# Performance work log

Hardware: AMD Instinct MI355X
Metric: run time of the kernel (lower is better)

Reference implementation:

```python
import jax, jax.numpy as jnp
import numpy as np

B, T, D, H = 4, 4096, 256, 64  # batch, seq, DIM_EMBEDDING (fixed constant), head_size


def setup_inputs() -> dict:
    key = jax.random.key(0)
    ks = jax.random.split(key, 6)
    x = jax.random.normal(ks[0], (B, T, D), dtype=jnp.float32)
    scale = jnp.float32(0.02)
    Wq = jax.random.normal(ks[1], (D, H), dtype=jnp.float32) * scale
    Wk = jax.random.normal(ks[2], (D, H), dtype=jnp.float32) * scale
    Wv = jax.random.normal(ks[3], (D, H), dtype=jnp.float32) * scale
    two_pi = jnp.float32(2.0 * np.pi)
    angles_x = jax.random.uniform(ks[4], (T, H // 4), dtype=jnp.float32, maxval=two_pi)
    angles_y = jax.random.uniform(ks[5], (T, H // 4), dtype=jnp.float32, maxval=two_pi)
    return {"x": x, "Wq": Wq, "Wk": Wk, "Wv": Wv, "angles_x": angles_x, "angles_y": angles_y}


def _rope_half(v, freqs):
    # v: (B, T, H/2) real; freqs: (T, H/4) complex64 (unit phasors)
    b, t, h = v.shape
    vc = v.astype(jnp.float32).reshape(b, t, h // 2, 2)
    vz = jax.lax.complex(vc[..., 0], vc[..., 1])         # (B, T, H/4)
    rz = vz * freqs[None]                                 # complex multiply per position
    out = jnp.stack([jnp.real(rz), jnp.imag(rz)], axis=-1)
    return out.reshape(b, t, h)


def _rope2d(v, fx, fy):
    vx, vy = jnp.split(v, 2, axis=-1)
    return jnp.concatenate([_rope_half(vx, fx), _rope_half(vy, fy)], axis=-1)


def reference(x, Wq, Wk, Wv, angles_x, angles_y):
    # complex unit phasors e^{i*theta}
    fx = jax.lax.complex(jnp.cos(angles_x), jnp.sin(angles_x))
    fy = jax.lax.complex(jnp.cos(angles_y), jnp.sin(angles_y))
    # original apply_rotary_embeddings is wrapped in @torch.no_grad -> detached
    q = jax.lax.stop_gradient(_rope2d(x @ Wq, fx, fy))
    k = jax.lax.stop_gradient(_rope2d(x @ Wk, fx, fy))
    v = x @ Wv
    C = x.shape[-1]  # NOTE: source scales by embedding dim (256), not head dim
    wei = jnp.einsum('bth,bsh->bts', q, k) / jnp.sqrt(jnp.float32(C))
    softwei = jax.nn.softmax(wei, axis=-1)  # no causal mask in source
    out = jnp.einsum('bts,bsh->bth', softwei, v)
    return out
```

## Files before the change

kernel.cpp:

```cpp
#include <hip/hip_runtime.h>

#define B_ 4
#define T_ 4096
#define D_ 256
#define H_ 64
#define NBT (B_ * T_)
#define NBTH (B_ * T_ * H_)

typedef __bf16 bf16x8 __attribute__((ext_vector_type(8)));
typedef float f32x4 __attribute__((ext_vector_type(4)));

__device__ __forceinline__ unsigned short f2bf(float f) {
  union { float f; unsigned int u; } v; v.f = f;
  unsigned int u = v.u;
  return (unsigned short)((u + 0x7fffu + ((u >> 16) & 1u)) >> 16);
}

#if __has_builtin(__builtin_amdgcn_cvt_pk_bf16_f32)
typedef __bf16 bf16x2_t __attribute__((ext_vector_type(2)));
__device__ __forceinline__ unsigned int pk2(float a, float b) {
  union { bf16x2_t v; unsigned int u; } c;
  c.v = __builtin_amdgcn_cvt_pk_bf16_f32(a, b);
  return c.u;
}
#else
__device__ __forceinline__ unsigned int pk2(float a, float b) {
  return (unsigned int)f2bf(a) | ((unsigned int)f2bf(b) << 16);
}
#endif

#if __has_builtin(__builtin_amdgcn_exp2f)
#define EXP2(x) __builtin_amdgcn_exp2f(x)
#else
#define EXP2(x) exp2f(x)
#endif

#define QSCALE 0.09016844f


__global__ __launch_bounds__(256) void prep_w_kernel(
    const float* __restrict__ Wq, const float* __restrict__ Wk,
    const float* __restrict__ Wv, unsigned short* __restrict__ wt) {
  const int m = blockIdx.x >> 2;
  const int cp = blockIdx.x & 3;
  const float* W = (m == 0) ? Wq : (m == 1) ? Wk : Wv;
  const float scale = (m == 0) ? QSCALE : 1.f;
  __shared__ __align__(16) unsigned short tile[64][72];
  int h = threadIdx.x & 63, dq = threadIdx.x >> 6;
  const int d0 = cp * 64;
  for (int dl = dq; dl < 64; dl += 4)
    tile[h][dl] = f2bf(W[(d0 + dl) * H_ + h] * scale);
  __syncthreads();
  int ht = threadIdx.x >> 6;
  int lane = threadIdx.x & 63, quad = lane >> 4, l16 = lane & 15;
#pragma unroll
  for (int cl = 0; cl < 2; ++cl) {
    int c = cp * 2 + cl;
    bf16x8 v = *(const bf16x8*)&tile[ht * 16 + l16][cl * 32 + quad * 8];
    *(bf16x8*)&wt[(((m * 4 + ht) * 8 + c) << 9) + lane * 8] = v;
  }
}

__global__ __launch_bounds__(192) void qkv_kernel(
    const float* __restrict__ x, const unsigned short* __restrict__ wt,
    const float* __restrict__ axg, const float* __restrict__ ayg,
    unsigned short* __restrict__ qo, unsigned short* __restrict__ ko,
    unsigned short* __restrict__ vt) {
  const int row0g = blockIdx.x * 16;
  const int tid = threadIdx.x;
  const int w = tid / 64, lane = tid & 63, quad = lane >> 4, l16 = lane & 15;

  __shared__ unsigned short xs[16][264];
  __shared__ unsigned short qkt[2][16][72];
  __shared__ unsigned short vsh[64][16];

  const float4* xb = (const float4*)(x + (size_t)row0g * D_);
  for (int i = tid; i < 1024; i += 192) {
    float4 v = xb[i];
    int r = i >> 6, c4 = (i & 63) << 2;
    *(unsigned int*)&xs[r][c4] = pk2(v.x, v.y);
    *(unsigned int*)&xs[r][c4 + 2] = pk2(v.z, v.w);
  }
  __syncthreads();

  bf16x8 xf[8];
#pragma unroll
  for (int c = 0; c < 8; ++c)
    xf[c] = *(const bf16x8*)&xs[l16][c * 32 + quad * 8];

  const unsigned short* wb = wt + (((size_t)w * 4) * 8 << 9);
  f32x4 acc[4];
#pragma unroll
  for (int ht = 0; ht < 4; ++ht) acc[ht] = (f32x4){0.f, 0.f, 0.f, 0.f};
#pragma unroll
  for (int c = 0; c < 8; ++c) {
#pragma unroll
    for (int ht = 0; ht < 4; ++ht) {
      bf16x8 wf = *(const bf16x8*)&wb[((ht * 8 + c) << 9) + lane * 8];
      acc[ht] = __builtin_amdgcn_mfma_f32_16x16x32_bf16(xf[c], wf, acc[ht],
                                                        0, 0, 0);
    }
  }

  const int row0loc = row0g & (T_ - 1);
  if (w < 2) {
    const float sgn = (l16 & 1) ? 1.f : -1.f;
#pragma unroll
    for (int ht = 0; ht < 4; ++ht) {
      int hh = ht * 16 + l16;
      int pidx = (hh & 31) >> 1;
      const float* ab = (hh >= 32) ? ayg : axg;
#pragma unroll
      for (int r = 0; r < 4; ++r) {
        int t = row0loc + quad * 4 + r;
        float s, c;
        __sincosf(ab[t * 16 + pidx], &s, &c);
        float val = acc[ht][r];
        float par = __shfl_xor(val, 1);
        qkt[w][quad * 4 + r][hh] = f2bf(val * c + sgn * par * s);
      }
    }
    asm volatile("s_waitcnt lgkmcnt(0)" ::: "memory");
    unsigned short* dst;
    size_t base;
    if (w == 0) {
      dst = qo;
      base = ((size_t)(row0g >> 4) * 2) << 9;
    } else {
      dst = ko;
      base = ((size_t)((row0g >> 6) * 8 + ((row0g >> 4) & 3) * 2)) << 9;
    }
#pragma unroll
    for (int half = 0; half < 2; ++half) {
      bf16x8 v = *(const bf16x8*)&qkt[w][l16][half * 32 + quad * 8];
      *(bf16x8*)&dst[base + half * 512 + lane * 8] = v;
    }
  } else {
#pragma unroll
    for (int ht = 0; ht < 4; ++ht)
#pragma unroll
      for (int r = 0; r < 4; ++r)
        vsh[ht * 16 + l16][quad * 4 + r] = f2bf(acc[ht][r]);
    asm volatile("s_waitcnt lgkmcnt(0)" ::: "memory");
    const int kvblk = row0g >> 6;
    const int mt = (row0g >> 4) & 3;
    const int half_v = mt >> 1, qlow = (mt & 1) * 2;
#pragma unroll
    for (int it = 0; it < 2; ++it) {
      int hhx = it * 2 + (quad >> 1);
      int qp = qlow + (quad & 1);
      bf16x8 v = *(const bf16x8*)&vsh[hhx * 16 + l16][(quad & 1) * 8];
      *(bf16x8*)&vt[((((size_t)kvblk * 4 + hhx) * 2 + half_v) << 9) +
                    (qp * 16 + l16) * 8] = v;
    }
  }
}

#define LDP 72

__global__ __launch_bounds__(256, 4) void attn_kernel(
    const unsigned short* __restrict__ qfg, const unsigned short* __restrict__ kfg,
    const unsigned short* __restrict__ vfg, float* __restrict__ opart,
    float* __restrict__ lpart, int kv_len) {
  const int split = blockIdx.x >> 7;
  const int rem = blockIdx.x & 127;
  const int b = rem >> 5;
  const int q0 = (rem & 31) * 128;
  const int tid = threadIdx.x;
  const int w = tid >> 6, lane = tid & 63, quad = lane >> 4, l16 = lane & 15;

  __shared__ unsigned short Ps[4][32 * LDP];

  bf16x8 qf[2][2];
#pragma unroll
  for (int u = 0; u < 2; ++u) {
    size_t rb = (size_t)(b * T_ + q0 + w * 32 + u * 16) >> 4;
#pragma unroll
    for (int half = 0; half < 2; ++half)
      qf[u][half] = *(const bf16x8*)&qfg[((rb * 2 + half) << 9) + lane * 8];
  }

  f32x4 oacc[2][4];
  float lsum[2] = {0.f, 0.f};
  const f32x4 vzero = {0.f, 0.f, 0.f, 0.f};
#pragma unroll
  for (int u = 0; u < 2; ++u)
#pragma unroll
    for (int hh = 0; hh < 4; ++hh) oacc[u][hh] = vzero;

  const int kvb0 = (b * T_ + split * kv_len) >> 6;
  const int nkvb = kv_len >> 6;

  for (int kb = 0; kb < nkvb; ++kb) {
    const unsigned short* kfb = kfg + ((size_t)(kvb0 + kb) << 12);
    const unsigned short* vfb = vfg + ((size_t)(kvb0 + kb) << 12);

#pragma unroll
    for (int mt = 0; mt < 4; ++mt) {
      bf16x8 k0 = *(const bf16x8*)&kfb[((mt * 2 + 0) << 9) + lane * 8];
      bf16x8 k1 = *(const bf16x8*)&kfb[((mt * 2 + 1) << 9) + lane * 8];
#pragma unroll
      for (int u = 0; u < 2; ++u) {
        f32x4 s = vzero;
        s = __builtin_amdgcn_mfma_f32_16x16x32_bf16(k0, qf[u][0], s, 0, 0, 0);
        s = __builtin_amdgcn_mfma_f32_16x16x32_bf16(k1, qf[u][1], s, 0, 0, 0);
        float p0 = EXP2(s[0]);
        float p1 = EXP2(s[1]);
        float p2 = EXP2(s[2]);
        float p3 = EXP2(s[3]);
        lsum[u] += (p0 + p1) + (p2 + p3);
        uint2 pk;
        pk.x = pk2(p0, p1);
        pk.y = pk2(p2, p3);
        *(uint2*)&Ps[w][(u * 16 + l16) * LDP + mt * 16 + quad * 4] = pk;
      }
    }
    asm volatile("s_waitcnt lgkmcnt(0)" ::: "memory");

    bf16x8 ap[2][2];
#pragma unroll
    for (int u = 0; u < 2; ++u)
#pragma unroll
      for (int half = 0; half < 2; ++half)
        ap[u][half] =
            *(const bf16x8*)&Ps[w][(u * 16 + l16) * LDP + half * 32 + quad * 8];

#pragma unroll
    for (int hh = 0; hh < 4; ++hh) {
      bf16x8 v0 = *(const bf16x8*)&vfb[((hh * 2 + 0) << 9) + lane * 8];
      bf16x8 v1 = *(const bf16x8*)&vfb[((hh * 2 + 1) << 9) + lane * 8];
#pragma unroll
      for (int u = 0; u < 2; ++u) {
        oacc[u][hh] =
            __builtin_amdgcn_mfma_f32_16x16x32_bf16(ap[u][0], v0, oacc[u][hh], 0, 0, 0);
        oacc[u][hh] =
            __builtin_amdgcn_mfma_f32_16x16x32_bf16(ap[u][1], v1, oacc[u][hh], 0, 0, 0);
      }
    }
  }

#pragma unroll
  for (int u = 0; u < 2; ++u) {
    size_t base = (size_t)(split * B_ + b) * T_ + q0 + w * 32 + u * 16;
#pragma unroll
    for (int r = 0; r < 4; ++r) {
      float* orow = opart + (base + quad * 4 + r) * H_;
#pragma unroll
      for (int hh = 0; hh < 4; ++hh) orow[hh * 16 + l16] = oacc[u][hh][r];
    }
    float l = lsum[u];
    l += __shfl_xor(l, 16);
    l += __shfl_xor(l, 32);
    if (quad == 0) lpart[base + l16] = l;
  }
}

__global__ __launch_bounds__(256) void combine_kernel(
    const float* __restrict__ opart, const float* __restrict__ lpart,
    float* __restrict__ out, int ns) {
  int idx = blockIdx.x * 256 + threadIdx.x;
  int bt = idx >> 4;
  float den = 0.f;
  float axx = 0.f, ayy = 0.f, azz = 0.f, aww = 0.f;
  for (int s = 0; s < ns; ++s) {
    den += lpart[s * NBT + bt];
    float4 o = ((const float4*)opart)[(size_t)s * (NBTH / 4) + idx];
    axx += o.x; ayy += o.y; azz += o.z; aww += o.w;
  }
  float inv = 1.f / den;
  float4 res;
  res.x = axx * inv; res.y = ayy * inv; res.z = azz * inv; res.w = aww * inv;
  ((float4*)out)[idx] = res;
}

extern "C" void kernel_launch(void* const* d_in, const int* in_sizes, int n_in,
                              void* d_out, int out_size, void* d_ws,
                              size_t ws_size, hipStream_t stream) {
  const float* x  = (const float*)d_in[0];
  const float* Wq = (const float*)d_in[1];
  const float* Wk = (const float*)d_in[2];
  const float* Wv = (const float*)d_in[3];
  const float* ax = (const float*)d_in[4];
  const float* ay = (const float*)d_in[5];
  float* out = (float*)d_out;

  unsigned short* qo = (unsigned short*)d_ws;
  unsigned short* ko = qo + NBTH;
  unsigned short* vt = ko + NBTH;
  unsigned short* wt = vt + NBTH;
  float* opart = (float*)(wt + 3 * H_ * D_);

  size_t fixed = (size_t)3 * NBTH * 2 + (size_t)3 * H_ * D_ * 2;
  int NS = (ws_size >= fixed + (size_t)8 * NBTH * 4 + (size_t)8 * NBT * 4 + 256)
               ? 8 : 4;
  float* lpart = opart + (size_t)NS * NBTH;

  prep_w_kernel<<<12, 256, 0, stream>>>(Wq, Wk, Wv, wt);
  qkv_kernel<<<NBT / 16, 192, 0, stream>>>(x, wt, ax, ay, qo, ko, vt);
  attn_kernel<<<NS * 128, 256, 0, stream>>>(qo, ko, vt, opart, lpart, T_ / NS);
  combine_kernel<<<NBTH / 4 / 256, 256, 0, stream>>>(opart, lpart, out, NS);
}
```

Before: 113.9 us.

## Double query rows per wave and prefetch next K tile into registers

Each wave now handles 64 query rows instead of 32, so every K/V fragment loaded from global memory feeds twice as many MFMAs. The grid is halved to keep the same total work. The K tile for the next KV block is loaded into registers during the current iteration, and V loads are hoisted ahead of the PV MFMAs, to hide global load latency. In exchange, register and LDS use go up and launch bounds drop to 2 blocks per CU, which lowers occupancy.

```diff
diff --git a/kernel.cpp b/kernel.cpp
--- a/kernel.cpp
+++ b/kernel.cpp
@@ -158,52 +158,61 @@
 
 #define LDP 72
 
-__global__ __launch_bounds__(256, 4) void attn_kernel(
+__global__ __launch_bounds__(256, 2) void attn_kernel(
     const unsigned short* __restrict__ qfg, const unsigned short* __restrict__ kfg,
     const unsigned short* __restrict__ vfg, float* __restrict__ opart,
     float* __restrict__ lpart, int kv_len) {
-  const int split = blockIdx.x >> 7;
-  const int rem = blockIdx.x & 127;
-  const int b = rem >> 5;
-  const int q0 = (rem & 31) * 128;
+  const int split = blockIdx.x >> 6;
+  const int rem = blockIdx.x & 63;
+  const int b = rem >> 4;
+  const int q0 = (rem & 15) * 256;
   const int tid = threadIdx.x;
   const int w = tid >> 6, lane = tid & 63, quad = lane >> 4, l16 = lane & 15;
 
-  __shared__ unsigned short Ps[4][32 * LDP];
-
-  bf16x8 qf[2][2];
-#pragma unroll
-  for (int u = 0; u < 2; ++u) {
-    size_t rb = (size_t)(b * T_ + q0 + w * 32 + u * 16) >> 4;
+  __shared__ unsigned short Ps[4][64 * LDP];
+
+  bf16x8 qf[4][2];
+#pragma unroll
+  for (int u = 0; u < 4; ++u) {
+    size_t rb = (size_t)(b * T_ + q0 + w * 64 + u * 16) >> 4;
 #pragma unroll
     for (int half = 0; half < 2; ++half)
       qf[u][half] = *(const bf16x8*)&qfg[((rb * 2 + half) << 9) + lane * 8];
   }
 
-  f32x4 oacc[2][4];
-  float lsum[2] = {0.f, 0.f};
+  f32x4 oacc[4][4];
+  float lsum[4] = {0.f, 0.f, 0.f, 0.f};
   const f32x4 vzero = {0.f, 0.f, 0.f, 0.f};
 #pragma unroll
-  for (int u = 0; u < 2; ++u)
+  for (int u = 0; u < 4; ++u)
 #pragma unroll
     for (int hh = 0; hh < 4; ++hh) oacc[u][hh] = vzero;
 
   const int kvb0 = (b * T_ + split * kv_len) >> 6;
   const int nkvb = kv_len >> 6;
 
+  bf16x8 kf[8];
+  {
+    const unsigned short* kfb = kfg + ((size_t)kvb0 << 12);
+#pragma unroll
+    for (int f = 0; f < 8; ++f)
+      kf[f] = *(const bf16x8*)&kfb[(f << 9) + lane * 8];
+  }
+
   for (int kb = 0; kb < nkvb; ++kb) {
-    const unsigned short* kfb = kfg + ((size_t)(kvb0 + kb) << 12);
     const unsigned short* vfb = vfg + ((size_t)(kvb0 + kb) << 12);
+    const int kbn = (kb + 1 < nkvb) ? (kb + 1) : kb;
+    const unsigned short* kfb_n = kfg + ((size_t)(kvb0 + kbn) << 12);
 
 #pragma unroll
     for (int mt = 0; mt < 4; ++mt) {
-      bf16x8 k0 = *(const bf16x8*)&kfb[((mt * 2 + 0) << 9) + lane * 8];
-      bf16x8 k1 = *(const bf16x8*)&kfb[((mt * 2 + 1) << 9) + lane * 8];
-#pragma unroll
-      for (int u = 0; u < 2; ++u) {
+#pragma unroll
+      for (int u = 0; u < 4; ++u) {
         f32x4 s = vzero;
-        s = __builtin_amdgcn_mfma_f32_16x16x32_bf16(k0, qf[u][0], s, 0, 0, 0);
-        s = __builtin_amdgcn_mfma_f32_16x16x32_bf16(k1, qf[u][1], s, 0, 0, 0);
+        s = __builtin_amdgcn_mfma_f32_16x16x32_bf16(kf[mt * 2 + 0], qf[u][0],
+                                                    s, 0, 0, 0);
+        s = __builtin_amdgcn_mfma_f32_16x16x32_bf16(kf[mt * 2 + 1], qf[u][1],
+                                                    s, 0, 0, 0);
         float p0 = EXP2(s[0]);
         float p1 = EXP2(s[1]);
         float p2 = EXP2(s[2]);
@@ -215,11 +224,20 @@
         *(uint2*)&Ps[w][(u * 16 + l16) * LDP + mt * 16 + quad * 4] = pk;
       }
     }
+
+    bf16x8 vf[8];
+#pragma unroll
+    for (int f = 0; f < 8; ++f)
+      vf[f] = *(const bf16x8*)&vfb[(f << 9) + lane * 8];
+#pragma unroll
+    for (int f = 0; f < 8; ++f)
+      kf[f] = *(const bf16x8*)&kfb_n[(f << 9) + lane * 8];
+
     asm volatile("s_waitcnt lgkmcnt(0)" ::: "memory");
 
-    bf16x8 ap[2][2];
-#pragma unroll
-    for (int u = 0; u < 2; ++u)
+    bf16x8 ap[4][2];
+#pragma unroll
+    for (int u = 0; u < 4; ++u)
 #pragma unroll
       for (int half = 0; half < 2; ++half)
         ap[u][half] =
@@ -227,21 +245,19 @@
 
 #pragma unroll
     for (int hh = 0; hh < 4; ++hh) {
-      bf16x8 v0 = *(const bf16x8*)&vfb[((hh * 2 + 0) << 9) + lane * 8];
-      bf16x8 v1 = *(const bf16x8*)&vfb[((hh * 2 + 1) << 9) + lane * 8];
-#pragma unroll
-      for (int u = 0; u < 2; ++u) {
-        oacc[u][hh] =
-            __builtin_amdgcn_mfma_f32_16x16x32_bf16(ap[u][0], v0, oacc[u][hh], 0, 0, 0);
-        oacc[u][hh] =
-            __builtin_amdgcn_mfma_f32_16x16x32_bf16(ap[u][1], v1, oacc[u][hh], 0, 0, 0);
+#pragma unroll
+      for (int u = 0; u < 4; ++u) {
+        oacc[u][hh] = __builtin_amdgcn_mfma_f32_16x16x32_bf16(
+            ap[u][0], vf[hh * 2 + 0], oacc[u][hh], 0, 0, 0);
+        oacc[u][hh] = __builtin_amdgcn_mfma_f32_16x16x32_bf16(
+            ap[u][1], vf[hh * 2 + 1], oacc[u][hh], 0, 0, 0);
       }
     }
   }
 
 #pragma unroll
-  for (int u = 0; u < 2; ++u) {
-    size_t base = (size_t)(split * B_ + b) * T_ + q0 + w * 32 + u * 16;
+  for (int u = 0; u < 4; ++u) {
+    size_t base = (size_t)(split * B_ + b) * T_ + q0 + w * 64 + u * 16;
 #pragma unroll
     for (int r = 0; r < 4; ++r) {
       float* orow = opart + (base + quad * 4 + r) * H_;
@@ -297,6 +313,6 @@
 
   prep_w_kernel<<<12, 256, 0, stream>>>(Wq, Wk, Wv, wt);
   qkv_kernel<<<NBT / 16, 192, 0, stream>>>(x, wt, ax, ay, qo, ko, vt);
-  attn_kernel<<<NS * 128, 256, 0, stream>>>(qo, ko, vt, opart, lpart, T_ / NS);
+  attn_kernel<<<NS * 64, 256, 0, stream>>>(qo, ko, vt, opart, lpart, T_ / NS);
   combine_kernel<<<NBTH / 4 / 256, 256, 0, stream>>>(opart, lpart, out, NS);
 }
```

Result: faster. 110.8 us (-2.7%).
